# Kernel tuning notes

Hardware: AMD Instinct MI355X
Metric: run time of the kernel (lower is better)

## Reference

```python
import jax, jax.numpy as jnp
from jax import lax
import numpy as np
import math

# ---- static hyperparameters (from init_kwargs) ----
NUM_RAY = 64
NUM_RAY2 = NUM_RAY * NUM_RAY
NUM_SAMPLE = 64
STEP = 1.0 / (NUM_SAMPLE - 1)
RK = 3                       # RK4Range: neighbor cube side
K = 64                       # Num_RIGuassKernel per axis
PH = (192, 192, 192)         # PhantomSize (D, H, W)
THETA_X, THETA_Y, THETA_Z = 0.1, 0.05, 0.02
CENTER = (0.5, 0.5, 0.5)

# ---- constant neighbor offsets and kernel-center grids (Process_Parameter) ----
half = (RK - 1) // 2
_r = np.arange(-half, half + 1)
Xr_np, Yr_np, Zr_np = np.meshgrid(_r, _r, _r)
XR = jnp.asarray(Xr_np.flatten().reshape(1, RK ** 3), dtype=jnp.float32)
YR = jnp.asarray(Yr_np.flatten().reshape(1, RK ** 3), dtype=jnp.float32)
ZR = jnp.asarray(Zr_np.flatten().reshape(1, RK ** 3), dtype=jnp.float32)
_c = np.linspace(0, 1, K, dtype='float32')
Xc_np, Yc_np, Zc_np = np.meshgrid(_c, _c, _c)
XC = jnp.asarray(Xc_np.flatten())
YC = jnp.asarray(Yc_np.flatten())
ZC = jnp.asarray(Zc_np.flatten())

# ---- rotation matrices (Theta2TransMatrix) ----
def _build_transmats():
    def ry(t):
        c, s = math.cos(t), math.sin(t)
        return np.array([[1, 0, 0, 0], [0, c, -s, 0], [0, s, c, 0], [0, 0, 0, 1]], dtype=np.float64)
    def rx(t):
        c, s = math.cos(t), math.sin(t)
        return np.array([[c, 0, -s, 0], [0, 1, 0, 0], [s, 0, c, 0], [0, 0, 0, 1]], dtype=np.float64)
    def rz(t):
        c, s = math.cos(t), math.sin(t)
        return np.array([[c, -s, 0, 0], [s, c, 0, 0], [0, 0, 1, 0], [0, 0, 0, 1]], dtype=np.float64)
    RY, RY_ = ry(-THETA_Y), ry(THETA_Y)
    RX, RX_ = rx(THETA_X), rx(-THETA_X)
    RZ, RZ_ = rz(-THETA_Z), rz(THETA_Z)
    cx, cy, cz = CENTER
    S1 = np.eye(4); S1[3, :3] = [-cx, -cy, -cz]
    S2 = np.eye(4); S2[3, :3] = [cx, cy, cz]
    M_crd = S1 @ RZ @ RY @ RX @ S2
    M_drv = RX_ @ RY_ @ RZ_
    return jnp.asarray(M_crd, dtype=jnp.float32), jnp.asarray(M_drv, dtype=jnp.float32)

M_CRD, M_DRV = _build_transmats()


def _indexdist(x, y, z, RI):
    # x,y,z: [N]; RI: [K^3, 2] -> Gaussian-kernel interpolated n and spatial derivatives
    X, Y, Z = x[:, None], y[:, None], z[:, None]
    Xn = jnp.clip(jnp.round(X * K) + XR, 0.0, K - 1.0)
    Yn = jnp.clip(jnp.round(Y * K) + YR, 0.0, K - 1.0)
    Zn = jnp.clip(jnp.round(Z * K) + ZR, 0.0, K - 1.0)
    lin = (K * K * Yn + K * Xn + Zn).astype(jnp.int32)   # [N, RK^3]
    dx = XC[lin] - X
    dy = YC[lin] - Y
    dz = ZC[lin] - Z
    A = RI[lin, 0]
    sig = RI[lin, 1]
    inv_s2 = 1.0 / (sig * sig)
    ni = jnp.exp(-(dx * dx + dy * dy + dz * dz) * 0.5 * inv_s2) + 2e-7
    norm = jnp.sum(ni, axis=1)
    nu = ni * A
    nx = jnp.sum(nu * dx * inv_s2, axis=1)
    ny = jnp.sum(nu * dy * inv_s2, axis=1)
    nz = jnp.sum(nu * dz * inv_s2, axis=1)
    ndx = jnp.sum(ni * dx * inv_s2, axis=1)
    ndy = jnp.sum(ni * dy * inv_s2, axis=1)
    ndz = jnp.sum(ni * dz * inv_s2, axis=1)
    nu_s = jnp.sum(nu, axis=1)
    n = nu_s / norm
    inv_norm2 = 1.0 / (norm * norm)
    nx = (norm * nx - nu_s * ndx) * inv_norm2
    ny = (norm * ny - nu_s * ndy) * inv_norm2
    nz = (norm * nz - nu_s * ndz) * inv_norm2
    return n, nx, ny, nz


def _rayeq(z0, xy0, RI):
    ones = jnp.ones_like(z0)
    t = jnp.stack([xy0[:, 2], xy0[:, 0], z0, ones], axis=1) @ M_CRD
    n, dndx_, dndy_, dndz_ = _indexdist(t[:, 1], t[:, 0], t[:, 2], RI)
    d = jnp.stack([dndy_, dndx_, dndz_, ones], axis=1) @ M_DRV
    dndx, dndz, dndy = d[:, 1], d[:, 2], d[:, 0]
    dX1 = xy0[:, 1]
    dX2 = (dndx - dndz * dX1) * (1.0 + dX1 * dX1) / n
    dY1 = xy0[:, 3]
    dY2 = (dndy - dndz * dY1) * (1.0 + dY1 * dY1) / n
    return jnp.stack([dX1, dX2, dY1, dY2], axis=1)


def _ray_tracing(xyz0, RI):
    def step_fn(xyz, _):
        deriv = _rayeq(xyz[:, 4], xyz[:, 0:4], RI)
        xyzi = jnp.concatenate([xyz[:, 0:4] + deriv * STEP, (xyz[:, 4] + STEP)[:, None]], axis=1)
        return xyzi, xyzi
    _, rest = lax.scan(step_fn, xyz0, None, length=NUM_SAMPLE - 1)
    return jnp.concatenate([xyz0[None], rest], axis=0)   # [S, N, 5]


def _resize_axis_linear(a, axis, out_len):
    # align_corners=True 1D linear resize along `axis`
    in_len = a.shape[axis]
    pos = jnp.linspace(0.0, in_len - 1.0, out_len)
    i0 = jnp.clip(jnp.floor(pos).astype(jnp.int32), 0, in_len - 2)
    w = (pos - i0.astype(pos.dtype)).astype(a.dtype)
    a0 = jnp.take(a, i0, axis=axis)
    a1 = jnp.take(a, i0 + 1, axis=axis)
    shape = [1] * a.ndim
    shape[axis] = out_len
    w = w.reshape(shape)
    return a0 * (1.0 - w) + a1 * w


def _grid_sample_3d(vol, gx, gy, gz):
    # torch F.grid_sample trilinear, align_corners=True, padding_mode='zeros'
    D, H, W = vol.shape
    ix = (gx + 1.0) * 0.5 * (W - 1)
    iy = (gy + 1.0) * 0.5 * (H - 1)
    iz = (gz + 1.0) * 0.5 * (D - 1)
    x0 = jnp.floor(ix); y0 = jnp.floor(iy); z0 = jnp.floor(iz)
    fx = ix - x0; fy = iy - y0; fz = iz - z0
    out = jnp.zeros_like(ix)
    for dz in (0, 1):
        for dyy in (0, 1):
            for dxx in (0, 1):
                xi = x0 + dxx; yi = y0 + dyy; zi = z0 + dz
                wgt = (jnp.where(dxx == 1, fx, 1.0 - fx)
                       * jnp.where(dyy == 1, fy, 1.0 - fy)
                       * jnp.where(dz == 1, fz, 1.0 - fz))
                inb = ((xi >= 0) & (xi <= W - 1) & (yi >= 0) & (yi <= H - 1)
                       & (zi >= 0) & (zi <= D - 1))
                xc = jnp.clip(xi, 0, W - 1).astype(jnp.int32)
                yc = jnp.clip(yi, 0, H - 1).astype(jnp.int32)
                zc = jnp.clip(zi, 0, D - 1).astype(jnp.int32)
                out = out + jnp.where(inb, wgt * vol[zc, yc, xc], 0.0)
    return out


def setup_inputs() -> dict:
    key = jax.random.key(0)
    k1, k2, k3, k4, k5 = jax.random.split(key, 5)
    Phantom = jax.random.uniform(k1, (1, 1) + PH, dtype=jnp.float32)
    A = jax.random.uniform(k2, (K ** 3, 1), dtype=jnp.float32) * 0.9 + 0.1
    sig = jax.random.uniform(k3, (K ** 3, 1), dtype=jnp.float32) * 0.8 + 0.2
    RefractionIndex = jnp.concatenate([A, sig], axis=1)
    xy = jax.random.uniform(k4, (NUM_RAY2, 2), dtype=jnp.float32) * 0.8 + 0.1
    slopes = jax.random.normal(k5, (NUM_RAY2, 2), dtype=jnp.float32) * 0.05
    z0 = jnp.zeros((NUM_RAY2, 1), dtype=jnp.float32)
    # layout [x, dx/dz, y, dy/dz, z]
    RayInit = jnp.concatenate([xy[:, :1], slopes[:, :1], xy[:, 1:], slopes[:, 1:], z0], axis=1)
    return {"Phantom": Phantom, "RefractionIndex": RefractionIndex, "RayInit": RayInit}


def reference(Phantom, RefractionIndex, RayInit):
    RayInit = RayInit.reshape(NUM_RAY2, 5)
    RI = RefractionIndex.reshape(K ** 3, 2)
    paths = _ray_tracing(RayInit, RI)          # [S, N, 5]
    paths = paths * 2.0 - 1.0
    # paths -> [3, R, R, S] mesh of (x, y, z) coordinates
    mesh = jnp.stack([
        paths[:, :, 0].T.reshape(NUM_RAY, NUM_RAY, NUM_SAMPLE),
        paths[:, :, 2].T.reshape(NUM_RAY, NUM_RAY, NUM_SAMPLE),
        paths[:, :, 4].T.reshape(NUM_RAY, NUM_RAY, NUM_SAMPLE),
    ], axis=0)
    # trilinear resize (align_corners=True) to PhantomSize
    for ax, out_len in zip((1, 2, 3), PH):
        mesh = _resize_axis_linear(mesh, ax, out_len)   # [3, D, H, W]
    vol = Phantom.reshape(PH)
    out = _grid_sample_3d(vol, mesh[0], mesh[1], mesh[2])
    return out.reshape((1, 1) + PH)
```

## Files before the change

### kernel.cpp

```cpp
#include <hip/hip_runtime.h>
#include <math.h>

#define NRAY2 4096
#define NSAMP 64
#define PHD 192
constexpr float STEP = 1.0f / 63.0f;

struct Mats { float crd[16]; float drv[16]; };

static void mat_mul4(const double* A, const double* B, double* C) {
    for (int i = 0; i < 4; ++i)
        for (int j = 0; j < 4; ++j) {
            double s = 0.0;
            for (int k = 0; k < 4; ++k) s += A[i*4+k] * B[k*4+j];
            C[i*4+j] = s;
        }
}

static void build_mats(Mats& M) {
    const double tx = 0.1, ty = 0.05, tz = 0.02;
    const double cx = 0.5, cy = 0.5, cz = 0.5;
    auto ry = [](double t, double* m) {
        double c = cos(t), s = sin(t);
        double v[16] = {1,0,0,0, 0,c,-s,0, 0,s,c,0, 0,0,0,1};
        for (int i = 0; i < 16; ++i) m[i] = v[i];
    };
    auto rx = [](double t, double* m) {
        double c = cos(t), s = sin(t);
        double v[16] = {c,0,-s,0, 0,1,0,0, s,0,c,0, 0,0,0,1};
        for (int i = 0; i < 16; ++i) m[i] = v[i];
    };
    auto rz = [](double t, double* m) {
        double c = cos(t), s = sin(t);
        double v[16] = {c,-s,0,0, s,c,0,0, 0,0,1,0, 0,0,0,1};
        for (int i = 0; i < 16; ++i) m[i] = v[i];
    };
    double RY[16], RY_[16], RX[16], RX_[16], RZ[16], RZ_[16];
    ry(-ty, RY); ry(ty, RY_);
    rx(tx, RX);  rx(-tx, RX_);
    rz(-tz, RZ); rz(tz, RZ_);
    double S1[16] = {1,0,0,0, 0,1,0,0, 0,0,1,0, -cx,-cy,-cz,1};
    double S2[16] = {1,0,0,0, 0,1,0,0, 0,0,1,0,  cx, cy, cz,1};
    double t1[16], t2[16], t3[16], Mc[16], Md[16];
    mat_mul4(S1, RZ, t1);
    mat_mul4(t1, RY, t2);
    mat_mul4(t2, RX, t3);
    mat_mul4(t3, S2, Mc);
    mat_mul4(RX_, RY_, t1);
    mat_mul4(t1, RZ_, Md);
    for (int i = 0; i < 16; ++i) { M.crd[i] = (float)Mc[i]; M.drv[i] = (float)Md[i]; }
}

__device__ __forceinline__ float red32(float x) {
    int t;
    t = __builtin_amdgcn_update_dpp(0, __float_as_int(x), 0x121, 0xF, 0xF, true);
    x += __int_as_float(t);
    t = __builtin_amdgcn_update_dpp(0, __float_as_int(x), 0x122, 0xF, 0xF, true);
    x += __int_as_float(t);
    t = __builtin_amdgcn_update_dpp(0, __float_as_int(x), 0x124, 0xF, 0xF, true);
    x += __int_as_float(t);
    t = __builtin_amdgcn_update_dpp(0, __float_as_int(x), 0x128, 0xF, 0xF, true);
    x += __int_as_float(t);
    t = __builtin_amdgcn_ds_swizzle(__float_as_int(x), 0x401F);
    x += __int_as_float(t);
    return x;
}

__global__ __launch_bounds__(256) void ray_trace_kernel(
    const float* __restrict__ RI,
    const float* __restrict__ RayInit,
    float* __restrict__ meshXT,
    float* __restrict__ meshYT,
    Mats M)
{
    const int tid = threadIdx.x;
    const int nb  = tid & 31;
    const int ray = blockIdx.x * 8 + (tid >> 5);
    const bool act = nb < 27;

    float xr = 0.f, yr = 0.f, zr = 0.f;
    if (act) {
        int a0 = nb / 9, a1 = (nb / 3) % 3, a2 = nb % 3;
        xr = (float)(a1 - 1);
        yr = (float)(a0 - 1);
        zr = (float)(a2 - 1);
    }

    float X  = RayInit[ray*5 + 0];
    float dX = RayInit[ray*5 + 1];
    float Y  = RayInit[ray*5 + 2];
    float dY = RayInit[ray*5 + 3];
    float z  = RayInit[ray*5 + 4];

    if (nb == 0) meshXT[ray] = X*2.0f - 1.0f;
    if (nb == 1) meshYT[ray] = Y*2.0f - 1.0f;

    auto prep = [&](float pX, float pY, float pz,
                    float& ox, float& oy, float& oz,
                    float& oXn, float& oYn, float& oZn) -> const float2* {
        float x  = pY*M.crd[1] + pX*M.crd[5] + pz*M.crd[9]  + M.crd[13];
        float y  = pY*M.crd[0] + pX*M.crd[4] + pz*M.crd[8]  + M.crd[12];
        float zz = pY*M.crd[2] + pX*M.crd[6] + pz*M.crd[10] + M.crd[14];
        float XnL = fminf(fmaxf(rintf(x *64.0f) + xr, 0.0f), 63.0f);
        float YnL = fminf(fmaxf(rintf(y *64.0f) + yr, 0.0f), 63.0f);
        float ZnL = fminf(fmaxf(rintf(zz*64.0f) + zr, 0.0f), 63.0f);
        int lin = ((int)YnL << 12) + ((int)XnL << 6) + (int)ZnL;
        ox = x; oy = y; oz = zz; oXn = XnL; oYn = YnL; oZn = ZnL;
        return (const float2*)RI + lin;
    };

    float cx_, cy_, cz_, Xn, Yn, Zn;
    float2 ri = *prep(X, Y, z, cx_, cy_, cz_, Xn, Yn, Zn);

    for (int s = 1; s < NSAMP; ++s) {
        float nX = X + dX*STEP, nY = Y + dY*STEP, nz = z + STEP;
        float ncx, ncy, ncz, nXn, nYn, nZn;
        float2 ri_n = *prep(nX, nY, nz, ncx, ncy, ncz, nXn, nYn, nZn);

        float dx = Xn*(1.0f/63.0f) - cx_;
        float dy = Yn*(1.0f/63.0f) - cy_;
        float dz = Zn*(1.0f/63.0f) - cz_;
        float inv_s2 = __builtin_amdgcn_rcpf(ri.y * ri.y);
        float e = __expf(-(dx*dx + dy*dy + dz*dz) * 0.5f * inv_s2) + 2e-7f;
        if (!act) e = 0.0f;
        float gdx = dx*inv_s2, gdy = dy*inv_s2, gdz = dz*inv_s2;
        float nu  = e * ri.x;

        float ni  = red32(e);
        float nuA = red32(nu);
        float sx  = red32(nu * gdx);
        float sy  = red32(nu * gdy);
        float sz  = red32(nu * gdz);
        float sdx = red32(e  * gdx);
        float sdy = red32(e  * gdy);
        float sdz = red32(e  * gdz);

        float r   = __builtin_amdgcn_rcpf(ni);
        float rn  = ni * __builtin_amdgcn_rcpf(nuA);
        float in2 = r * r;
        float gx_ = (ni*sx - nuA*sdx) * in2;
        float gy_ = (ni*sy - nuA*sdy) * in2;
        float gz_ = (ni*sz - nuA*sdz) * in2;

        float dndx = gy_*M.drv[1] + gx_*M.drv[5] + gz_*M.drv[9]  + M.drv[13];
        float dndy = gy_*M.drv[0] + gx_*M.drv[4] + gz_*M.drv[8]  + M.drv[12];
        float dndz = gy_*M.drv[2] + gx_*M.drv[6] + gz_*M.drv[10] + M.drv[14];

        float dX2 = (dndx - dndz*dX) * (1.0f + dX*dX) * rn;
        float dY2 = (dndy - dndz*dY) * (1.0f + dY*dY) * rn;

        X = nX; Y = nY; z = nz;
        dX += dX2 * STEP;
        dY += dY2 * STEP;

        if (nb == 0) meshXT[s*NRAY2 + ray] = X*2.0f - 1.0f;
        if (nb == 1) meshYT[s*NRAY2 + ray] = Y*2.0f - 1.0f;

        cx_ = ncx; cy_ = ncy; cz_ = ncz;
        Xn = nXn; Yn = nYn; Zn = nZn;
        ri = ri_n;
    }
}

typedef _Float16 h16;
typedef _Float16 h16v4 __attribute__((ext_vector_type(4)));

__global__ __launch_bounds__(1024) void sample_kernel(
    const float* __restrict__ vol,
    const float* __restrict__ meshXT,
    const float* __restrict__ meshYT,
    float* __restrict__ out)
{
    __shared__ h16    plane_h[PHD*PHD];
    __shared__ float2 slice[64*64];
    __shared__ float  wTab[PHD];
    __shared__ int    iTab[PHD];

    const int tid = threadIdx.x;
    const int blk = blockIdx.x;
    const int c = (blk >> 3) + 24 * (blk & 7);

    if (tid < PHD) {
        float p = tid * (63.0f / 191.0f);
        int i0 = min((int)p, 62);
        iTab[tid] = i0;
        wTab[tid] = p - (float)i0;
    }

    {
        const float4* src = (const float4*)(vol + c * (PHD*PHD));
        h16v4* dst = (h16v4*)plane_h;
        #pragma unroll
        for (int k = 0; k < (PHD*PHD/4)/1024; ++k) {
            float4 v = src[tid + k*1024];
            h16v4 hv = {(h16)v.x, (h16)v.y, (h16)v.z, (h16)v.w};
            dst[tid + k*1024] = hv;
        }
    }

    float ps = c * (63.0f / 191.0f);
    int s0 = min((int)ps, 62);
    float wc = ps - (float)s0, wc0 = 1.0f - wc;
    {
        const float* x0 = meshXT + s0*NRAY2;
        const float* x1 = meshXT + (s0+1)*NRAY2;
        const float* y0 = meshYT + s0*NRAY2;
        const float* y1 = meshYT + (s0+1)*NRAY2;
        #pragma unroll
        for (int k = 0; k < 4096/1024; ++k) {
            int t = tid + k*1024;
            slice[t] = make_float2(x0[t]*wc0 + x1[t]*wc,
                                   y0[t]*wc0 + y1[t]*wc);
        }
    }
    __syncthreads();

    int a = tid / PHD, b = tid % PHD;
    #pragma unroll 2
    for (int k = 0; k < (PHD*PHD)/1024; ++k) {
        int i0 = iTab[a]; float wa = wTab[a];
        int j0 = iTab[b]; float wb = wTab[b];

        float2 s00 = slice[i0*64 + j0];
        float2 s01 = slice[i0*64 + j0 + 1];
        float2 s10 = slice[(i0+1)*64 + j0];
        float2 s11 = slice[(i0+1)*64 + j0 + 1];

        float wb0 = 1.0f - wb, wa0 = 1.0f - wa;
        float gx = (s00.x*wb0 + s01.x*wb)*wa0 + (s10.x*wb0 + s11.x*wb)*wa;
        float gy = (s00.y*wb0 + s01.y*wb)*wa0 + (s10.y*wb0 + s11.y*wb)*wa;

        float ix = (gx + 1.0f) * 0.5f * 191.0f;
        float iy = (gy + 1.0f) * 0.5f * 191.0f;
        float x0f = floorf(ix); float fx = ix - x0f;
        float y0f = floorf(iy); float fy = iy - y0f;

        float acc = 0.0f;
        #pragma unroll
        for (int dyy = 0; dyy < 2; ++dyy) {
            #pragma unroll
            for (int dxx = 0; dxx < 2; ++dxx) {
                float xi = x0f + (float)dxx;
                float yi = y0f + (float)dyy;
                bool inb = (xi >= 0.0f) && (xi <= 191.0f) &&
                           (yi >= 0.0f) && (yi <= 191.0f);
                int xc = min(max((int)xi, 0), PHD - 1);
                int yc = min(max((int)yi, 0), PHD - 1);
                float w = (dxx ? fx : 1.0f - fx) * (dyy ? fy : 1.0f - fy);
                float val = (float)plane_h[yc*PHD + xc];
                acc += inb ? w * val : 0.0f;
            }
        }
        out[(a*PHD + b)*PHD + c] = acc;

        a += 5; b += 64;
        if (b >= PHD) { b -= PHD; a += 1; }
    }
}

extern "C" void kernel_launch(void* const* d_in, const int* in_sizes, int n_in,
                              void* d_out, int out_size, void* d_ws, size_t ws_size,
                              hipStream_t stream)
{
    const float* Phantom = (const float*)d_in[0];
    const float* RI      = (const float*)d_in[1];
    const float* RayInit = (const float*)d_in[2];
    float* out = (float*)d_out;

    float* meshXT = (float*)d_ws;
    float* meshYT = meshXT + NRAY2 * NSAMP;

    Mats M;
    build_mats(M);

    ray_trace_kernel<<<NRAY2/8, 256, 0, stream>>>(RI, RayInit, meshXT, meshYT, M);
    sample_kernel<<<PHD, 1024, 0, stream>>>(Phantom, meshXT, meshYT, out);
}
```

Measured before the change: 163.8 us.

## Write sample output contiguously to workspace, then transpose with tiled kernel

The sampling kernel previously wrote each output with a stride of 192 floats along the c axis, so stores were uncoalesced. It can now write each plane contiguously into a workspace buffer, and a separate shared-memory tiled transpose kernel reorders the data into the final layout. This path runs only when the workspace is large enough, and it adds a full extra read and write of the 28 MB volume plus one more launch. The ray-trace index computation also switches to fmed3 clamps and a float-based linear index.

Result: faster. 156.3 us (-4.6%).

```diff
diff --git a/kernel.cpp b/kernel.cpp
--- a/kernel.cpp
+++ b/kernel.cpp
@@ -4,6 +4,7 @@
 #define NRAY2 4096
 #define NSAMP 64
 #define PHD 192
+#define PLANE (PHD*PHD)
 constexpr float STEP = 1.0f / 63.0f;
 
 struct Mats { float crd[16]; float drv[16]; };
@@ -101,10 +102,10 @@
         float x  = pY*M.crd[1] + pX*M.crd[5] + pz*M.crd[9]  + M.crd[13];
         float y  = pY*M.crd[0] + pX*M.crd[4] + pz*M.crd[8]  + M.crd[12];
         float zz = pY*M.crd[2] + pX*M.crd[6] + pz*M.crd[10] + M.crd[14];
-        float XnL = fminf(fmaxf(rintf(x *64.0f) + xr, 0.0f), 63.0f);
-        float YnL = fminf(fmaxf(rintf(y *64.0f) + yr, 0.0f), 63.0f);
-        float ZnL = fminf(fmaxf(rintf(zz*64.0f) + zr, 0.0f), 63.0f);
-        int lin = ((int)YnL << 12) + ((int)XnL << 6) + (int)ZnL;
+        float XnL = __builtin_amdgcn_fmed3f(rintf(x *64.0f) + xr, 0.0f, 63.0f);
+        float YnL = __builtin_amdgcn_fmed3f(rintf(y *64.0f) + yr, 0.0f, 63.0f);
+        float ZnL = __builtin_amdgcn_fmed3f(rintf(zz*64.0f) + zr, 0.0f, 63.0f);
+        int lin = (int)(YnL*4096.0f + XnL*64.0f + ZnL);
         ox = x; oy = y; oz = zz; oXn = XnL; oYn = YnL; oZn = ZnL;
         return (const float2*)RI + lin;
     };
@@ -169,9 +170,10 @@
     const float* __restrict__ vol,
     const float* __restrict__ meshXT,
     const float* __restrict__ meshYT,
-    float* __restrict__ out)
+    float* __restrict__ outDst,
+    int transposed)
 {
-    __shared__ h16    plane_h[PHD*PHD];
+    __shared__ h16    plane_h[PLANE];
     __shared__ float2 slice[64*64];
     __shared__ float  wTab[PHD];
     __shared__ int    iTab[PHD];
@@ -188,10 +190,10 @@
     }
 
     {
-        const float4* src = (const float4*)(vol + c * (PHD*PHD));
+        const float4* src = (const float4*)(vol + c * PLANE);
         h16v4* dst = (h16v4*)plane_h;
         #pragma unroll
-        for (int k = 0; k < (PHD*PHD/4)/1024; ++k) {
+        for (int k = 0; k < (PLANE/4)/1024; ++k) {
             float4 v = src[tid + k*1024];
             h16v4 hv = {(h16)v.x, (h16)v.y, (h16)v.z, (h16)v.w};
             dst[tid + k*1024] = hv;
@@ -217,7 +219,7 @@
 
     int a = tid / PHD, b = tid % PHD;
     #pragma unroll 2
-    for (int k = 0; k < (PHD*PHD)/1024; ++k) {
+    for (int k = 0; k < PLANE/1024; ++k) {
         int i0 = iTab[a]; float wa = wTab[a];
         int j0 = iTab[b]; float wb = wTab[b];
 
@@ -251,11 +253,37 @@
                 acc += inb ? w * val : 0.0f;
             }
         }
-        out[(a*PHD + b)*PHD + c] = acc;
+
+        if (transposed) {
+            outDst[c*PLANE + tid + k*1024] = acc;
+        } else {
+            outDst[(a*PHD + b)*PHD + c] = acc;
+        }
 
         a += 5; b += 64;
         if (b >= PHD) { b -= PHD; a += 1; }
     }
+}
+
+__global__ __launch_bounds__(256) void transpose_kernel(
+    const float* __restrict__ outT, float* __restrict__ out)
+{
+    __shared__ float t[32][33];
+    const int a  = blockIdx.z;
+    const int b0 = blockIdx.x * 32;
+    const int c0 = blockIdx.y * 32;
+    const int tx = threadIdx.x, ty = threadIdx.y;
+
+    const float* src = outT + (size_t)(c0 + ty) * PLANE + a*PHD + b0 + tx;
+    #pragma unroll
+    for (int j = 0; j < 4; ++j)
+        t[ty + 8*j][tx] = src[(size_t)(8*j) * PLANE];
+    __syncthreads();
+
+    float* dst = out + (size_t)a * PLANE + (size_t)(b0 + ty) * PHD + c0 + tx;
+    #pragma unroll
+    for (int j = 0; j < 4; ++j)
+        dst[(size_t)(8*j) * PHD] = t[tx][ty + 8*j];
 }
 
 extern "C" void kernel_launch(void* const* d_in, const int* in_sizes, int n_in,
@@ -269,10 +297,20 @@
 
     float* meshXT = (float*)d_ws;
     float* meshYT = meshXT + NRAY2 * NSAMP;
+    float* outT   = meshYT + NRAY2 * NSAMP;
+
+    const size_t need = (size_t)(2 * NRAY2 * NSAMP + PHD*PLANE) * sizeof(float);
+    const int use_transpose = (ws_size >= need) ? 1 : 0;
 
     Mats M;
     build_mats(M);
 
     ray_trace_kernel<<<NRAY2/8, 256, 0, stream>>>(RI, RayInit, meshXT, meshYT, M);
-    sample_kernel<<<PHD, 1024, 0, stream>>>(Phantom, meshXT, meshYT, out);
-}
+
+    if (use_transpose) {
+        sample_kernel<<<PHD, 1024, 0, stream>>>(Phantom, meshXT, meshYT, outT, 1);
+        transpose_kernel<<<dim3(6, 6, PHD), dim3(32, 8), 0, stream>>>(outT, out);
+    } else {
+        sample_kernel<<<PHD, 1024, 0, stream>>>(Phantom, meshXT, meshYT, out, 0);
+    }
+}
```
